# Kernel optimization log

Measured on AMD Instinct MI355X. Metric: run time of the kernel, lower is better.

The kernel has to match this reference:

```python
import jax, jax.numpy as jnp
import numpy as np

B, N, L, D = 1, 128, 256, 256   # batch, num_seqs, seq_len, msa_dim
P, H = 128, 8                   # pair_dim, num_heads
DH = D // H                     # head_dim


def setup_inputs() -> dict:
    key = jax.random.key(0)
    ks = jax.random.split(key, 7)
    msa = jax.random.normal(ks[0], (B, N, L, D), dtype=jnp.float32)
    pair = jax.random.normal(ks[1], (B, L, L, P), dtype=jnp.float32)
    mask = jax.random.randint(ks[2], (B, N, L), 0, 2) > 0  # bool key mask
    w_qkv = jax.random.normal(ks[3], (D, 3 * D), dtype=jnp.float32) * (D ** -0.5)
    w_pb = jax.random.normal(ks[4], (P, H), dtype=jnp.float32) * (P ** -0.5)
    b_pb = jnp.zeros((H,), dtype=jnp.float32)
    w_out = jax.random.normal(ks[5], (D, D), dtype=jnp.float32) * (D ** -0.5)
    b_out = jnp.zeros((D,), dtype=jnp.float32)
    return {"msa": msa, "pair": pair, "mask": mask, "w_qkv": w_qkv,
            "w_pb": w_pb, "b_pb": b_pb, "w_out": w_out, "b_out": b_out}


def reference(msa, pair, mask, w_qkv, w_pb, b_pb, w_out, b_out):
    b, n, l, d = msa.shape
    scaling = DH ** -0.5
    qkv = msa @ w_qkv                                   # [b,n,l,3d]
    qkv = qkv.reshape(b, n, l, 3, H, DH)
    q, k, v = qkv[..., 0, :, :], qkv[..., 1, :, :], qkv[..., 2, :, :]  # [b,n,l,h,dh]
    pair_bias = (pair @ w_pb + b_pb)                    # [b,l,l,h]
    pair_bias = jnp.transpose(pair_bias, (0, 3, 1, 2))  # [b,h,l,l]
    # scores: [b,n,h,l,l]
    dots = jnp.einsum('bnqhd,bnkhd->bnhqk', q, k) * scaling
    dots = dots + pair_bias[:, None]                    # broadcast over num_seqs
    dots = jnp.where(mask[:, :, None, None, :], dots, -jnp.inf)  # mask keys
    attn = jax.nn.softmax(dots, axis=-1)
    out = jnp.einsum('bnhqk,bnkhd->bnqhd', attn, v)     # [b,n,l,h,dh]
    out = out.reshape(b, n, l, d)
    return out @ w_out + b_out
```

## Files before the change

kernel.cpp:

```cpp
#include <hip/hip_runtime.h>
#include <hip/hip_bf16.h>

#define NN 128
#define LL 256
#define DD 256
#define PP 128
#define HH 8
#define DHH 32

typedef __bf16 bf16x8 __attribute__((ext_vector_type(8)));
typedef short s16x4 __attribute__((ext_vector_type(4)));
typedef float f32x4 __attribute__((ext_vector_type(4)));
typedef unsigned int u32x2 __attribute__((ext_vector_type(2)));

__global__ __launch_bounds__(256) void cvt_bf16(
    const float* __restrict__ src, __hip_bfloat16* __restrict__ dst, int n) {
  for (int i = (blockIdx.x * 256 + threadIdx.x) * 4; i < n; i += gridDim.x * 1024) {
    float4 v = *(const float4*)(src + i);
    ushort4 o;
    o.x = __bfloat16_as_ushort(__float2bfloat16(v.x));
    o.y = __bfloat16_as_ushort(__float2bfloat16(v.y));
    o.z = __bfloat16_as_ushort(__float2bfloat16(v.z));
    o.w = __bfloat16_as_ushort(__float2bfloat16(v.w));
    *(ushort4*)(dst + i) = o;
  }
}

__global__ __launch_bounds__(256) void transpose_cvt(
    const float* __restrict__ src, __hip_bfloat16* __restrict__ dst,
    int K, int N) {
  __shared__ float t[32][33];
  int n0 = blockIdx.x * 32, k0 = blockIdx.y * 32;
  int tx = threadIdx.x & 31, ty = threadIdx.x >> 5;
  for (int i = 0; i < 4; ++i) {
    int ky = ty + i * 8;
    t[ky][tx] = src[(size_t)(k0 + ky) * N + n0 + tx];
  }
  __syncthreads();
  for (int i = 0; i < 4; ++i) {
    int ny = ty + i * 8;
    dst[(size_t)(n0 + ny) * K + k0 + tx] = __float2bfloat16(t[tx][ny]);
  }
}

#define MODE_I32 0
#define MODE_I8 1
#define MODE_BF16 2
#define MODE_F32 3

__global__ __launch_bounds__(256) void mask_expand(
    const unsigned char* __restrict__ mraw, int* __restrict__ mout) {
  __shared__ int s_or1, s_or2, s_or3, s_max, s_mode;
  int tid = threadIdx.x;
  if (tid == 0) { s_or1 = 0; s_or2 = 0; s_or3 = 0; s_max = 0; }
  __syncthreads();
  int or1 = 0, or2 = 0, or3 = 0, mx = 0;
  for (int j = tid; j < 4096; j += 256) {
    int b = mraw[j];
    mx = mx > b ? mx : b;
    int r = j & 3;
    if (r == 1) or1 |= b;
    else if (r == 2) or2 |= b;
    else if (r == 3) or3 |= b;
  }
  atomicOr(&s_or1, or1); atomicOr(&s_or2, or2); atomicOr(&s_or3, or3);
  atomicMax(&s_max, mx);
  __syncthreads();
  if (tid == 0) {
    int mode;
    if (s_max <= 1) mode = ((s_or1 | s_or2 | s_or3) == 0) ? MODE_I32 : MODE_I8;
    else            mode = (s_or1 != 0) ? MODE_BF16 : MODE_F32;
    s_mode = mode;
  }
  __syncthreads();
  int mode = s_mode;
  int i0 = blockIdx.x * 1024;
  for (int i = i0 + tid; i < i0 + 1024; i += 256) {
    int v;
    if (mode == MODE_I32)       v = ((const int*)mraw)[i] != 0;
    else if (mode == MODE_I8)   v = mraw[i] != 0;
    else if (mode == MODE_BF16) v = ((const unsigned short*)mraw)[i] != 0;
    else                        v = ((const unsigned int*)mraw)[i] != 0;
    mout[i] = v;
  }
}

#define GEMM_MAINLOOP(Aptr, Btptr)                                            \
  __shared__ __align__(16) __hip_bfloat16 Asm[128 * 32];                      \
  __shared__ __align__(16) __hip_bfloat16 Bsm[128 * 32];                      \
  int tid = threadIdx.x;                                                      \
  int lane = tid & 63;                                                        \
  int wv = tid >> 6;                                                          \
  int wm = (wv >> 1) * 64, wn = (wv & 1) * 64;                                \
  int lr = lane & 15, quad = lane >> 4;                                       \
  int bm = blockIdx.x, bn = blockIdx.y;                                       \
  f32x4 acc[4][4];                                                            \
  for (int i = 0; i < 4; ++i)                                                 \
    for (int j = 0; j < 4; ++j) acc[i][j] = (f32x4){0.f, 0.f, 0.f, 0.f};      \
  for (int ks = 0; ks < 8; ++ks) {                                            \
    int k0 = ks * 32;                                                         \
    if (ks) __syncthreads();                                                  \
    for (int i = 0; i < 2; ++i) {                                             \
      int c = tid + i * 256;                                                  \
      int row = c >> 2, cc = c & 3;                                           \
      ((uint4*)Asm)[c] =                                                      \
          *(const uint4*)(Aptr + ((size_t)(bm * 128 + row)) * 256 + k0 + cc * 8); \
      ((uint4*)Bsm)[c] =                                                      \
          *(const uint4*)(Btptr + ((size_t)(bn * 128 + row)) * 256 + k0 + cc * 8); \
    }                                                                         \
    __syncthreads();                                                          \
    bf16x8 af[4], bfr[4];                                                     \
    for (int mi = 0; mi < 4; ++mi)                                            \
      af[mi] = *(const bf16x8*)&Asm[(wm + mi * 16 + lr) * 32 + quad * 8];     \
    for (int ni = 0; ni < 4; ++ni)                                            \
      bfr[ni] = *(const bf16x8*)&Bsm[(wn + ni * 16 + lr) * 32 + quad * 8];    \
    for (int mi = 0; mi < 4; ++mi)                                            \
      for (int ni = 0; ni < 4; ++ni)                                          \
        acc[mi][ni] = __builtin_amdgcn_mfma_f32_16x16x32_bf16(                \
            af[mi], bfr[ni], acc[mi][ni], 0, 0, 0);                           \
  }

__global__ __launch_bounds__(256) void qkv_gemm_mfma(
    const __hip_bfloat16* __restrict__ A,
    const __hip_bfloat16* __restrict__ Bt,
    __hip_bfloat16* __restrict__ qb,
    __hip_bfloat16* __restrict__ kb,
    __hip_bfloat16* __restrict__ vb) {
  GEMM_MAINLOOP(A, Bt)
  for (int mi = 0; mi < 4; ++mi) {
    for (int ni = 0; ni < 4; ++ni) {
      int gcol = bn * 128 + wn + ni * 16 + lr;
      int t = gcol >> 8, rem = gcol & 255;
      int h = rem >> 5, dh = rem & 31;
      for (int r = 0; r < 4; ++r) {
        int grow = bm * 128 + wm + mi * 16 + quad * 4 + r;
        int n = grow >> 8, l = grow & 255;
        __hip_bfloat16 val = __float2bfloat16(acc[mi][ni][r]);
        if (t == 0)
          qb[(size_t)(((n * HH + h) * LL + l)) * DHH + dh] = val;
        else if (t == 1)
          kb[(size_t)(((n * HH + h) * LL + l)) * DHH + dh] = val;
        else
          vb[(size_t)(((n * HH + h) * DHH + dh)) * LL + l] = val;
      }
    }
  }
}

__global__ __launch_bounds__(256) void out_gemm_mfma(
    const __hip_bfloat16* __restrict__ A,
    const __hip_bfloat16* __restrict__ Bt,
    const float* __restrict__ bout,
    float* __restrict__ C) {
  GEMM_MAINLOOP(A, Bt)
  for (int mi = 0; mi < 4; ++mi) {
    for (int ni = 0; ni < 4; ++ni) {
      int gcol = bn * 128 + wn + ni * 16 + lr;
      float bo = bout[gcol];
      for (int r = 0; r < 4; ++r) {
        int grow = bm * 128 + wm + mi * 16 + quad * 4 + r;
        C[(size_t)grow * 256 + gcol] = acc[mi][ni][r] + bo;
      }
    }
  }
}

__global__ __launch_bounds__(256) void pair_bias_kernel(
    const float* __restrict__ pair,
    const float* __restrict__ w_pb,
    const float* __restrict__ b_pb,
    float* __restrict__ bias) {
  __shared__ float wp[128][9];
  __shared__ float rows[32][129];
  int tid = threadIdx.x;
  for (int i = 0; i < 4; ++i) {
    int e = tid + i * 256;
    wp[e >> 3][e & 7] = w_pb[e];
  }
  int row0 = blockIdx.x * 32;
  const float* src = pair + (size_t)row0 * PP;
  for (int i = 0; i < 16; ++i) {
    int e = tid + i * 256;
    int r = e >> 7, c = e & 127;
    rows[r][c] = src[r * 128 + c];
  }
  __syncthreads();
  int h = tid >> 5, rl = tid & 31;
  float acc = b_pb[h] - 12.0f;
  for (int p = 0; p < 128; ++p)
    acc += rows[rl][p] * wp[p][h];
  int row = row0 + rl;
  int i = row >> 8, j = row & 255;
  bias[((size_t)(h * LL + i)) * LL + j] = acc;
}

__global__ __launch_bounds__(256) void attn_mfma(
    const __hip_bfloat16* __restrict__ qb,
    const __hip_bfloat16* __restrict__ kb,
    const __hip_bfloat16* __restrict__ vbt,
    const float* __restrict__ biasQ,
    const int* __restrict__ mask,
    __hip_bfloat16* __restrict__ ao) {
  int bx = blockIdx.x;
  int h = bx >> 7, n = bx & 127;
  int nh = n * HH + h;
  int tid = threadIdx.x, lane = tid & 63, wv = tid >> 6;
  int lr = lane & 15, quad = lane >> 4;
  int wm = wv * 64;
  size_t base = (size_t)nh * (LL * DHH);

  const __hip_bfloat16* qp = qb + base;
  const __hip_bfloat16* kp = kb + base;
  const __hip_bfloat16* vp = vbt + base;
  const float* bQ = biasQ + (size_t)h * LL * LL;
  const int* mrow = mask + n * LL;

  const float scale = 0.17677669529663687f;

  bf16x8 aq[4];
#pragma unroll
  for (int mi = 0; mi < 4; ++mi)
    aq[mi] = *(const bf16x8*)(qp + (size_t)(wm + mi * 16 + lr) * DHH + quad * 8);

  float lsum[4] = {0.f, 0.f, 0.f, 0.f};
  f32x4 o_acc[4][2];
#pragma unroll
  for (int mi = 0; mi < 4; ++mi)
#pragma unroll
    for (int no = 0; no < 2; ++no) o_acc[mi][no] = (f32x4){0.f, 0.f, 0.f, 0.f};

#pragma unroll
  for (int kt = 0; kt < 4; ++kt) {
    int j0 = kt * 64;
    bf16x8 bk[4];
#pragma unroll
    for (int nj = 0; nj < 4; ++nj)
      bk[nj] = *(const bf16x8*)(kp + (size_t)(j0 + nj * 16 + lr) * DHH + quad * 8);
    s16x4 av[4][2];
#pragma unroll
    for (int nj = 0; nj < 4; ++nj)
#pragma unroll
      for (int no = 0; no < 2; ++no)
        av[nj][no] = *(const s16x4*)(vp + (size_t)(no * 16 + lr) * LL +
                                     j0 + nj * 16 + quad * 4);
    f32x4 mw[4];
#pragma unroll
    for (int nj = 0; nj < 4; ++nj) {
      int4 m4 = *(const int4*)(mrow + j0 + nj * 16 + quad * 4);
      mw[nj][0] = m4.x ? 1.f : 0.f;
      mw[nj][1] = m4.y ? 1.f : 0.f;
      mw[nj][2] = m4.z ? 1.f : 0.f;
      mw[nj][3] = m4.w ? 1.f : 0.f;
    }

#pragma unroll
    for (int mi = 0; mi < 4; ++mi) {
      f32x4 s[4];
#pragma unroll
      for (int nj = 0; nj < 4; ++nj)
        s[nj] = __builtin_amdgcn_mfma_f32_16x16x32_bf16(
            bk[nj], aq[mi], (f32x4){0.f, 0.f, 0.f, 0.f}, 0, 0, 0);

      const float* brow = bQ + (size_t)(wm + mi * 16 + lr) * LL + j0;
#pragma unroll
      for (int nj = 0; nj < 4; ++nj) {
        f32x4 b4 = *(const f32x4*)(brow + nj * 16 + quad * 4);
        float p0 = __expf(fmaf(s[nj][0], scale, b4[0])) * mw[nj][0];
        float p1 = __expf(fmaf(s[nj][1], scale, b4[1])) * mw[nj][1];
        float p2 = __expf(fmaf(s[nj][2], scale, b4[2])) * mw[nj][2];
        float p3 = __expf(fmaf(s[nj][3], scale, b4[3])) * mw[nj][3];
        lsum[mi] += (p0 + p1) + (p2 + p3);
        unsigned lo = ((unsigned)__bfloat16_as_ushort(__float2bfloat16(p1)) << 16) |
                      (unsigned)__bfloat16_as_ushort(__float2bfloat16(p0));
        unsigned hi = ((unsigned)__bfloat16_as_ushort(__float2bfloat16(p3)) << 16) |
                      (unsigned)__bfloat16_as_ushort(__float2bfloat16(p2));
        u32x2 pu = {lo, hi};
        s16x4 pb = __builtin_bit_cast(s16x4, pu);
#pragma unroll
        for (int no = 0; no < 2; ++no)
          o_acc[mi][no] = __builtin_amdgcn_mfma_f32_16x16x16bf16_1k(
              av[nj][no], pb, o_acc[mi][no], 0, 0, 0);
      }
    }
  }

#pragma unroll
  for (int mi = 0; mi < 4; ++mi) {
    float ls = lsum[mi];
    ls += __shfl_xor(ls, 16);
    ls += __shfl_xor(ls, 32);
    float inv = (ls > 0.f) ? 1.f / ls : 0.f;
    int q = wm + mi * 16 + lr;
#pragma unroll
    for (int no = 0; no < 2; ++no) {
      f32x4 o = o_acc[mi][no];
      ushort4 w;
      w.x = __bfloat16_as_ushort(__float2bfloat16(o[0] * inv));
      w.y = __bfloat16_as_ushort(__float2bfloat16(o[1] * inv));
      w.z = __bfloat16_as_ushort(__float2bfloat16(o[2] * inv));
      w.w = __bfloat16_as_ushort(__float2bfloat16(o[3] * inv));
      *(ushort4*)(ao + (size_t)n * (LL * DD) + (size_t)q * DD +
                  h * DHH + no * 16 + quad * 4) = w;
    }
  }
}

extern "C" void kernel_launch(void* const* d_in, const int* in_sizes, int n_in,
                              void* d_out, int out_size, void* d_ws, size_t ws_size,
                              hipStream_t stream) {
  const float* msa   = (const float*)d_in[0];
  const float* pair  = (const float*)d_in[1];
  const unsigned char* mask = (const unsigned char*)d_in[2];
  const float* w_qkv = (const float*)d_in[3];
  const float* w_pb  = (const float*)d_in[4];
  const float* b_pb  = (const float*)d_in[5];
  const float* w_out = (const float*)d_in[6];
  const float* b_out = (const float*)d_in[7];
  float* out = (float*)d_out;

  char* ws = (char*)d_ws;
  __hip_bfloat16* qb      = (__hip_bfloat16*)(ws);
  __hip_bfloat16* kb      = (__hip_bfloat16*)(ws + 16777216);
  __hip_bfloat16* vb      = (__hip_bfloat16*)(ws + 33554432);
  __hip_bfloat16* msa_c   = (__hip_bfloat16*)(ws + 50331648);
  __hip_bfloat16* ao      = (__hip_bfloat16*)(ws + 50331648);
  float*          bias    = (float*)(ws + 67108864);
  __hip_bfloat16* wqkv_t  = (__hip_bfloat16*)(ws + 71303168);
  __hip_bfloat16* wout_t  = (__hip_bfloat16*)(ws + 71696384);
  int*            msk     = (int*)(ws + 71827456);

  mask_expand<<<32, 256, 0, stream>>>(mask, msk);
  cvt_bf16<<<1024, 256, 0, stream>>>(msa, msa_c, NN * LL * DD);
  transpose_cvt<<<dim3(24, 8), 256, 0, stream>>>(w_qkv, wqkv_t, 256, 768);
  transpose_cvt<<<dim3(8, 8), 256, 0, stream>>>(w_out, wout_t, 256, 256);

  qkv_gemm_mfma<<<dim3(256, 6), 256, 0, stream>>>(msa_c, wqkv_t, qb, kb, vb);
  pair_bias_kernel<<<2048, 256, 0, stream>>>(pair, w_pb, b_pb, bias);
  attn_mfma<<<1024, 256, 0, stream>>>(qb, kb, vb, bias, msk, ao);
  out_gemm_mfma<<<dim3(256, 2), 256, 0, stream>>>(ao, wout_t, b_out, out);
}
```

Before: 256.9 us.

## Precompute exp(bias) in bf16, prefetch attention operands, use direct-to-LDS GEMM loads

The pair bias kernel now stores exp(bias) as bf16 instead of fp32 bias, so the attention kernel multiplies exp2(score) by the stored factor. This halves bias traffic and removes one add from the inner loop. The attention kernel double-buffers its K, V, mask and exp-bias register loads one step ahead to hide global latency, and it requests 2 blocks per CU through launch bounds. The mask is pre-expanded to floats, and the GEMM mainloop uses global_load_lds to copy tiles straight into LDS. Storing exp(bias) in bf16 costs some precision, and the extra prefetch buffers raise register pressure.

Result: slower. 301.8 us (+17.5%).

```diff
diff --git a/kernel.cpp b/kernel.cpp
--- a/kernel.cpp
+++ b/kernel.cpp
@@ -12,6 +12,12 @@
 typedef short s16x4 __attribute__((ext_vector_type(4)));
 typedef float f32x4 __attribute__((ext_vector_type(4)));
 typedef unsigned int u32x2 __attribute__((ext_vector_type(2)));
+
+__device__ __forceinline__ void gload_lds16(const void* g, void* l) {
+  __builtin_amdgcn_global_load_lds(
+      (const __attribute__((address_space(1))) void*)g,
+      (__attribute__((address_space(3))) void*)l, 16, 0, 0);
+}
 
 __global__ __launch_bounds__(256) void cvt_bf16(
     const float* __restrict__ src, __hip_bfloat16* __restrict__ dst, int n) {
@@ -49,7 +55,7 @@
 #define MODE_F32 3
 
 __global__ __launch_bounds__(256) void mask_expand(
-    const unsigned char* __restrict__ mraw, int* __restrict__ mout) {
+    const unsigned char* __restrict__ mraw, float* __restrict__ mout) {
   __shared__ int s_or1, s_or2, s_or3, s_max, s_mode;
   int tid = threadIdx.x;
   if (tid == 0) { s_or1 = 0; s_or2 = 0; s_or3 = 0; s_max = 0; }
@@ -81,7 +87,7 @@
     else if (mode == MODE_I8)   v = mraw[i] != 0;
     else if (mode == MODE_BF16) v = ((const unsigned short*)mraw)[i] != 0;
     else                        v = ((const unsigned int*)mraw)[i] != 0;
-    mout[i] = v;
+    mout[i] = v ? 1.f : 0.f;
   }
 }
 
@@ -103,10 +109,11 @@
     for (int i = 0; i < 2; ++i) {                                             \
       int c = tid + i * 256;                                                  \
       int row = c >> 2, cc = c & 3;                                           \
-      ((uint4*)Asm)[c] =                                                      \
-          *(const uint4*)(Aptr + ((size_t)(bm * 128 + row)) * 256 + k0 + cc * 8); \
-      ((uint4*)Bsm)[c] =                                                      \
-          *(const uint4*)(Btptr + ((size_t)(bn * 128 + row)) * 256 + k0 + cc * 8); \
+      int ldsbase = (wv * 64 + i * 256) * 8;      \
+      gload_lds16(Aptr + ((size_t)(bm * 128 + row)) * 256 + k0 + cc * 8,      \
+                  Asm + ldsbase);                                             \
+      gload_lds16(Btptr + ((size_t)(bn * 128 + row)) * 256 + k0 + cc * 8,     \
+                  Bsm + ldsbase);                                             \
     }                                                                         \
     __syncthreads();                                                          \
     bf16x8 af[4], bfr[4];                                                     \
@@ -169,7 +176,7 @@
     const float* __restrict__ pair,
     const float* __restrict__ w_pb,
     const float* __restrict__ b_pb,
-    float* __restrict__ bias) {
+    __hip_bfloat16* __restrict__ expb) {
   __shared__ float wp[128][9];
   __shared__ float rows[32][129];
   int tid = threadIdx.x;
@@ -191,15 +198,15 @@
     acc += rows[rl][p] * wp[p][h];
   int row = row0 + rl;
   int i = row >> 8, j = row & 255;
-  bias[((size_t)(h * LL + i)) * LL + j] = acc;
-}
-
-__global__ __launch_bounds__(256) void attn_mfma(
+  expb[((size_t)(h * LL + i)) * LL + j] = __float2bfloat16(__expf(acc));
+}
+
+__global__ __launch_bounds__(256, 2) void attn_mfma(
     const __hip_bfloat16* __restrict__ qb,
     const __hip_bfloat16* __restrict__ kb,
     const __hip_bfloat16* __restrict__ vbt,
-    const float* __restrict__ biasQ,
-    const int* __restrict__ mask,
+    const __hip_bfloat16* __restrict__ expb,
+    const float* __restrict__ maskf,
     __hip_bfloat16* __restrict__ ao) {
   int bx = blockIdx.x;
   int h = bx >> 7, n = bx & 127;
@@ -212,16 +219,46 @@
   const __hip_bfloat16* qp = qb + base;
   const __hip_bfloat16* kp = kb + base;
   const __hip_bfloat16* vp = vbt + base;
-  const float* bQ = biasQ + (size_t)h * LL * LL;
-  const int* mrow = mask + n * LL;
-
-  const float scale = 0.17677669529663687f;
+  const __hip_bfloat16* ep = expb + (size_t)h * LL * LL;
+  const float* mrow = maskf + n * LL;
+
+  const float cs = 0.17677669529663687f * 1.4426950408889634f;
 
   bf16x8 aq[4];
 #pragma unroll
   for (int mi = 0; mi < 4; ++mi)
     aq[mi] = *(const bf16x8*)(qp + (size_t)(wm + mi * 16 + lr) * DHH + quad * 8);
 
+  bf16x8 bk[2][4];
+  s16x4 av[2][4][2];
+  f32x4 mw[2][4];
+  uint2 eb[2][4];
+
+#define LOADKT(B, KT)                                                         \
+  do {                                                                        \
+    int j0_ = (KT) * 64;                                                      \
+    _Pragma("unroll") for (int nj = 0; nj < 4; ++nj)                          \
+        bk[B][nj] =                                                           \
+        *(const bf16x8*)(kp + (size_t)(j0_ + nj * 16 + lr) * DHH + quad * 8); \
+    _Pragma("unroll") for (int nj = 0; nj < 4; ++nj)                          \
+        _Pragma("unroll") for (int no = 0; no < 2; ++no)                      \
+        av[B][nj][no] = *(const s16x4*)(vp + (size_t)(no * 16 + lr) * LL +    \
+                                        j0_ + nj * 16 + quad * 4);            \
+    _Pragma("unroll") for (int nj = 0; nj < 4; ++nj)                          \
+        mw[B][nj] = *(const f32x4*)(mrow + j0_ + nj * 16 + quad * 4);         \
+  } while (0)
+
+#define LOADEB(B, KT, MI)                                                     \
+  do {                                                                        \
+    const __hip_bfloat16* er_ =                                               \
+        ep + (size_t)(wm + (MI) * 16 + lr) * LL + (KT) * 64;                  \
+    _Pragma("unroll") for (int nj = 0; nj < 4; ++nj)                          \
+        eb[B][nj] = *(const uint2*)(er_ + nj * 16 + quad * 4);                \
+  } while (0)
+
+  LOADKT(0, 0);
+  LOADEB(0, 0, 0);
+
   float lsum[4] = {0.f, 0.f, 0.f, 0.f};
   f32x4 o_acc[4][2];
 #pragma unroll
@@ -231,44 +268,33 @@
 
 #pragma unroll
   for (int kt = 0; kt < 4; ++kt) {
-    int j0 = kt * 64;
-    bf16x8 bk[4];
-#pragma unroll
-    for (int nj = 0; nj < 4; ++nj)
-      bk[nj] = *(const bf16x8*)(kp + (size_t)(j0 + nj * 16 + lr) * DHH + quad * 8);
-    s16x4 av[4][2];
-#pragma unroll
-    for (int nj = 0; nj < 4; ++nj)
-#pragma unroll
-      for (int no = 0; no < 2; ++no)
-        av[nj][no] = *(const s16x4*)(vp + (size_t)(no * 16 + lr) * LL +
-                                     j0 + nj * 16 + quad * 4);
-    f32x4 mw[4];
-#pragma unroll
-    for (int nj = 0; nj < 4; ++nj) {
-      int4 m4 = *(const int4*)(mrow + j0 + nj * 16 + quad * 4);
-      mw[nj][0] = m4.x ? 1.f : 0.f;
-      mw[nj][1] = m4.y ? 1.f : 0.f;
-      mw[nj][2] = m4.z ? 1.f : 0.f;
-      mw[nj][3] = m4.w ? 1.f : 0.f;
-    }
+    const int cur = kt & 1, nxt = cur ^ 1;
+    if (kt < 3) LOADKT(nxt, kt + 1);
 
 #pragma unroll
     for (int mi = 0; mi < 4; ++mi) {
+      const int ec = mi & 1, en = ec ^ 1;
+      if (mi < 3) LOADEB(en, kt, mi + 1);
+      else if (kt < 3) LOADEB(en, kt + 1, 0);
+
       f32x4 s[4];
 #pragma unroll
       for (int nj = 0; nj < 4; ++nj)
         s[nj] = __builtin_amdgcn_mfma_f32_16x16x32_bf16(
-            bk[nj], aq[mi], (f32x4){0.f, 0.f, 0.f, 0.f}, 0, 0, 0);
-
-      const float* brow = bQ + (size_t)(wm + mi * 16 + lr) * LL + j0;
+            bk[cur][nj], aq[mi], (f32x4){0.f, 0.f, 0.f, 0.f}, 0, 0, 0);
+
 #pragma unroll
       for (int nj = 0; nj < 4; ++nj) {
-        f32x4 b4 = *(const f32x4*)(brow + nj * 16 + quad * 4);
-        float p0 = __expf(fmaf(s[nj][0], scale, b4[0])) * mw[nj][0];
-        float p1 = __expf(fmaf(s[nj][1], scale, b4[1])) * mw[nj][1];
-        float p2 = __expf(fmaf(s[nj][2], scale, b4[2])) * mw[nj][2];
-        float p3 = __expf(fmaf(s[nj][3], scale, b4[3])) * mw[nj][3];
+        uint2 e = eb[ec][nj];
+        f32x4 m4 = mw[cur][nj];
+        float em0 = __uint_as_float(e.x << 16) * m4[0];
+        float em1 = __uint_as_float(e.x & 0xffff0000u) * m4[1];
+        float em2 = __uint_as_float(e.y << 16) * m4[2];
+        float em3 = __uint_as_float(e.y & 0xffff0000u) * m4[3];
+        float p0 = exp2f(s[nj][0] * cs) * em0;
+        float p1 = exp2f(s[nj][1] * cs) * em1;
+        float p2 = exp2f(s[nj][2] * cs) * em2;
+        float p3 = exp2f(s[nj][3] * cs) * em3;
         lsum[mi] += (p0 + p1) + (p2 + p3);
         unsigned lo = ((unsigned)__bfloat16_as_ushort(__float2bfloat16(p1)) << 16) |
                       (unsigned)__bfloat16_as_ushort(__float2bfloat16(p0));
@@ -279,7 +305,7 @@
 #pragma unroll
         for (int no = 0; no < 2; ++no)
           o_acc[mi][no] = __builtin_amdgcn_mfma_f32_16x16x16bf16_1k(
-              av[nj][no], pb, o_acc[mi][no], 0, 0, 0);
+              av[cur][nj][no], pb, o_acc[mi][no], 0, 0, 0);
       }
     }
   }
@@ -303,6 +329,8 @@
                   h * DHH + no * 16 + quad * 4) = w;
     }
   }
+#undef LOADKT
+#undef LOADEB
 }
 
 extern "C" void kernel_launch(void* const* d_in, const int* in_sizes, int n_in,
@@ -324,10 +352,10 @@
   __hip_bfloat16* vb      = (__hip_bfloat16*)(ws + 33554432);
   __hip_bfloat16* msa_c   = (__hip_bfloat16*)(ws + 50331648);
   __hip_bfloat16* ao      = (__hip_bfloat16*)(ws + 50331648);
-  float*          bias    = (float*)(ws + 67108864);
+  __hip_bfloat16* expb    = (__hip_bfloat16*)(ws + 67108864);
   __hip_bfloat16* wqkv_t  = (__hip_bfloat16*)(ws + 71303168);
   __hip_bfloat16* wout_t  = (__hip_bfloat16*)(ws + 71696384);
-  int*            msk     = (int*)(ws + 71827456);
+  float*          msk     = (float*)(ws + 71827456);
 
   mask_expand<<<32, 256, 0, stream>>>(mask, msk);
   cvt_bf16<<<1024, 256, 0, stream>>>(msa, msa_c, NN * LL * DD);
@@ -335,7 +363,7 @@
   transpose_cvt<<<dim3(8, 8), 256, 0, stream>>>(w_out, wout_t, 256, 256);
 
   qkv_gemm_mfma<<<dim3(256, 6), 256, 0, stream>>>(msa_c, wqkv_t, qb, kb, vb);
-  pair_bias_kernel<<<2048, 256, 0, stream>>>(pair, w_pb, b_pb, bias);
-  attn_mfma<<<1024, 256, 0, stream>>>(qb, kb, vb, bias, msk, ao);
+  pair_bias_kernel<<<2048, 256, 0, stream>>>(pair, w_pb, b_pb, expb);
+  attn_mfma<<<1024, 256, 0, stream>>>(qb, kb, vb, expb, msk, ao);
   out_gemm_mfma<<<dim3(256, 2), 256, 0, stream>>>(ao, wout_t, b_out, out);
 }
```
